# Kernel optimization log

Hardware: AMD Instinct MI355X
Metric: run time of the kernel (lower is better)

## Reference

```python
import jax, jax.numpy as jnp
import numpy as np

N_CODEBOOKS = 4
CODEBOOK_SIZE = 1024
CODEBOOK_DIM = 8
INPUT_DIM = 512
EPS_NORM = 1e-12  # F.normalize eps
EPS_SCALE = 1e-8


def _normalize(x, eps=EPS_NORM):
    n = jnp.linalg.norm(x, axis=-1, keepdims=True)
    return x / jnp.maximum(n, eps)


def _wn_weight(v, g):
    # weight-norm 1x1 conv weight: v [out, in], g [out]
    return g[:, None] * v / jnp.maximum(jnp.linalg.norm(v, axis=1, keepdims=True), EPS_NORM)


def _vq_step(residual, v_in, g_in, b_in, v_out, g_out, b_out, cb):
    # residual: [B, D, T]
    sg = jax.lax.stop_gradient
    w_in = _wn_weight(v_in, g_in)                                   # [cd, D]
    z_e = jnp.einsum('od,bdt->bot', w_in, residual) + b_in[None, :, None]  # [B, cd, T]

    # nearest-code search on L2-normalized vectors (same argmin as the cdist form)
    enc = jnp.transpose(z_e, (0, 2, 1))                             # [B, T, cd]
    sim = jnp.einsum('btd,kd->btk', _normalize(enc), _normalize(cb))
    idx = jnp.argmax(sim, axis=-1)                                  # [B, T]
    q_tok = cb[idx]                                                 # [B, T, cd]
    z_q_pre = jnp.transpose(q_tok, (0, 2, 1))                       # [B, cd, T]

    commit = jnp.mean((z_e - sg(z_q_pre)) ** 2, axis=(1, 2))        # [B]
    codeb = jnp.mean((z_q_pre - sg(z_e)) ** 2, axis=(1, 2))         # [B]

    # rotation trick: z_q = scale * (I - 2 r r^T + 2 q_n e_n^T) z_e, R/scale stop-grad
    e = enc                                                         # [B, T, cd]
    e_n = sg(_normalize(e))
    q_n = sg(_normalize(q_tok))
    r = sg(_normalize(e_n + q_n))
    scale = sg(jnp.linalg.norm(q_tok, axis=-1, keepdims=True)
               / jnp.maximum(jnp.linalg.norm(e, axis=-1, keepdims=True), EPS_SCALE))
    re = jnp.sum(r * e, axis=-1, keepdims=True)
    ene = jnp.sum(e_n * e, axis=-1, keepdims=True)
    z_rot = scale * (e - 2.0 * r * re + 2.0 * q_n * ene)            # [B, T, cd]
    z_q = jnp.transpose(z_rot, (0, 2, 1))                           # [B, cd, T]

    w_out = _wn_weight(v_out, g_out)                                # [D, cd]
    z_q_i = jnp.einsum('od,bdt->bot', w_out, z_q) + b_out[None, :, None]  # [B, D, T]
    return z_q_i, commit, codeb, idx


def setup_inputs() -> dict:
    key = jax.random.key(0)
    ks = jax.random.split(key, 8)
    B, D, T = 16, INPUT_DIM, 4096
    nq, K, cd = N_CODEBOOKS, CODEBOOK_SIZE, CODEBOOK_DIM
    return {
        'z': jax.random.normal(ks[0], (B, D, T), dtype=jnp.float32),
        'in_proj_v': jax.random.normal(ks[1], (nq, cd, D), dtype=jnp.float32) * (1.0 / np.sqrt(D)),
        'in_proj_g': jnp.ones((nq, cd), dtype=jnp.float32),
        'in_proj_b': jnp.zeros((nq, cd), dtype=jnp.float32),
        'out_proj_v': jax.random.normal(ks[2], (nq, D, cd), dtype=jnp.float32) * (1.0 / np.sqrt(cd)),
        'out_proj_g': jnp.ones((nq, D), dtype=jnp.float32),
        'out_proj_b': jnp.zeros((nq, D), dtype=jnp.float32),
        'codebooks': jax.random.normal(ks[3], (nq, K, cd), dtype=jnp.float32),
    }


def reference(z, in_proj_v, in_proj_g, in_proj_b, out_proj_v, out_proj_g, out_proj_b, codebooks):
    # eval-mode RVQ forward: all N_CODEBOOKS codebooks active (mask all ones)
    z_q = jnp.zeros_like(z)
    residual = z
    commitment_loss = jnp.float32(0.0)
    codebook_loss = jnp.float32(0.0)
    codes = []
    for i in range(N_CODEBOOKS):
        z_q_i, commit_i, codeb_i, idx_i = _vq_step(
            residual, in_proj_v[i], in_proj_g[i], in_proj_b[i],
            out_proj_v[i], out_proj_g[i], out_proj_b[i], codebooks[i])
        z_q = z_q + z_q_i
        residual = residual - z_q_i
        commitment_loss = commitment_loss + jnp.mean(commit_i)
        codebook_loss = codebook_loss + jnp.mean(codeb_i)
        codes.append(idx_i)
    return z_q, jnp.stack(codes, axis=0), commitment_loss, codebook_loss
```

## Files before the change

kernel.cpp:

```cpp
#include <hip/hip_runtime.h>
#include <cstddef>

#define NQ 4
#define KCODES 1024
#define CD 8
#define DIM 512
#define BATCH 16
#define TLEN 4096
#define TT 16
#define RPAD 17
#define NTHREADS 512

#define WS_WIN  0
#define WS_WOUT (NQ * DIM * CD)
#define WS_CBN  (2 * NQ * DIM * CD)
#define OUT_ZQ 0
#define OUT_CODES ((size_t)BATCH * DIM * TLEN)
#define OUT_LOSS (OUT_CODES + (size_t)NQ * BATCH * TLEN)

__global__ void rvq_zero(float* out) {
  out[OUT_LOSS] = 0.f;
  out[OUT_LOSS + 1] = 0.f;
}

__global__ void rvq_prep(const float* __restrict__ inv, const float* __restrict__ ing,
                         const float* __restrict__ outv, const float* __restrict__ outg,
                         const float* __restrict__ cb, float* __restrict__ ws) {
  const int blk = blockIdx.x, tid = threadIdx.x;
  if (blk < 32) {
    const int i = blk >> 3, o = blk & 7;
    const float* v = inv + (size_t)(i * CD + o) * DIM;
    const float a = v[tid], b = v[tid + 256];
    float s = a * a + b * b;
    #pragma unroll
    for (int off = 32; off >= 1; off >>= 1) s += __shfl_xor(s, off);
    __shared__ float red[4];
    if ((tid & 63) == 0) red[tid >> 6] = s;
    __syncthreads();
    const float nrm = fmaxf(sqrtf(red[0] + red[1] + red[2] + red[3]), 1e-12f);
    const float g = ing[i * CD + o];
    ws[WS_WIN + (size_t)((i * DIM + tid) * CD) + o] = (g * a) / nrm;
    ws[WS_WIN + (size_t)((i * DIM + tid + 256) * CD) + o] = (g * b) / nrm;
  } else {
    const int rid = (blk - 32) * 256 + tid;
    if (rid < NQ * DIM) {
      const float* v = outv + (size_t)rid * CD;
      float vv[8]; float n2 = 0.f;
      #pragma unroll
      for (int o = 0; o < 8; ++o) { vv[o] = v[o]; n2 += vv[o] * vv[o]; }
      const float nrm = fmaxf(sqrtf(n2), 1e-12f);
      const float g = outg[rid];
      #pragma unroll
      for (int o = 0; o < 8; ++o) ws[WS_WOUT + (size_t)rid * CD + o] = (g * vv[o]) / nrm;
    } else {
      const int k = rid - NQ * DIM;
      const float* v = cb + (size_t)k * CD;
      float vv[8]; float n2 = 0.f;
      #pragma unroll
      for (int o = 0; o < 8; ++o) { vv[o] = v[o]; n2 += vv[o] * vv[o]; }
      const float nrm = fmaxf(sqrtf(n2), 1e-12f);
      #pragma unroll
      for (int o = 0; o < 8; ++o) ws[WS_CBN + (size_t)k * CD + o] = vv[o] / nrm;
    }
  }
}

__launch_bounds__(NTHREADS, 8)
__global__ void rvq_main(const float* __restrict__ z,
                         const float* __restrict__ b_in, const float* __restrict__ b_out,
                         const float* __restrict__ cb, const float* __restrict__ ws,
                         float* __restrict__ out) {
  __shared__ float res[DIM * RPAD];
  __shared__ float part[8 * TT * 9];
  __shared__ float sc[8 * TT];
  __shared__ int   idl[8 * TT];

  const int tid = threadIdx.x;
  const int bb = blockIdx.x >> 8;
  const int t0 = (blockIdx.x & 255) * TT;
  const float* zb = z + (size_t)bb * DIM * TLEN + t0;

  {
    const int q = tid & 3, d0 = tid >> 2;
    #pragma unroll
    for (int p = 0; p < 4; ++p) {
      const int d = d0 + p * 128;
      const float4 v = *(const float4*)(zb + (size_t)d * TLEN + q * 4);
      float* rp = res + d * RPAD + q * 4;
      rp[0] = v.x; rp[1] = v.y; rp[2] = v.z; rp[3] = v.w;
    }
  }
  __syncthreads();

  const int t  = tid & 15;
  const int dc = tid >> 4;
  const int w  = tid >> 6;
  float loss_acc = 0.f;

  for (int i = 0; i < NQ; ++i) {
    float acc[8] = {0,0,0,0,0,0,0,0};
    {
      const float* wp = ws + WS_WIN + (size_t)(i * DIM + dc * 16) * CD;
      const float* rp = res + dc * 16 * RPAD + t;
      #pragma unroll
      for (int j = 0; j < 16; ++j) {
        const float r = rp[j * RPAD];
        const float4 w0 = *(const float4*)(wp + j * 8);
        const float4 w1 = *(const float4*)(wp + j * 8 + 4);
        acc[0] += w0.x * r; acc[1] += w0.y * r; acc[2] += w0.z * r; acc[3] += w0.w * r;
        acc[4] += w1.x * r; acc[5] += w1.y * r; acc[6] += w1.z * r; acc[7] += w1.w * r;
      }
    }
    #pragma unroll
    for (int o = 0; o < 8; ++o) {
      acc[o] += __shfl_xor(acc[o], 16);
      acc[o] += __shfl_xor(acc[o], 32);
    }
    if ((tid & 63) < 16) {
      float* pp = part + (w * TT + t) * 9;
      #pragma unroll
      for (int o = 0; o < 8; ++o) pp[o] = acc[o];
    }
    __syncthreads();

    float e[8];
    #pragma unroll
    for (int o = 0; o < 8; ++o) e[o] = b_in[i * CD + o];
    #pragma unroll
    for (int w2 = 0; w2 < 8; ++w2) {
      const float* pp = part + (w2 * TT + t) * 9;
      #pragma unroll
      for (int o = 0; o < 8; ++o) e[o] += pp[o];
    }
    float ne2 = 0.f;
    #pragma unroll
    for (int o = 0; o < 8; ++o) ne2 += e[o] * e[o];
    const float ne = sqrtf(ne2);

    float best = -1e30f; int bk = 0;
    {
      const float* cp = ws + WS_CBN + (size_t)(i * KCODES + dc * 32) * CD;
      #pragma unroll 4
      for (int k = 0; k < 32; ++k) {
        const float4 c0 = *(const float4*)(cp + k * 8);
        const float4 c1 = *(const float4*)(cp + k * 8 + 4);
        const float s = e[0]*c0.x + e[1]*c0.y + e[2]*c0.z + e[3]*c0.w
                      + e[4]*c1.x + e[5]*c1.y + e[6]*c1.z + e[7]*c1.w;
        if (s > best) { best = s; bk = dc * 32 + k; }
      }
    }
    #pragma unroll
    for (int off = 16; off <= 32; off <<= 1) {
      const float s2 = __shfl_xor(best, off);
      const int   k2 = __shfl_xor(bk, off);
      if (s2 > best || (s2 == best && k2 < bk)) { best = s2; bk = k2; }
    }
    if ((tid & 63) < 16) { sc[w * TT + t] = best; idl[w * TT + t] = bk; }
    __syncthreads();
    best = -1e30f; bk = KCODES;
    #pragma unroll
    for (int w2 = 0; w2 < 8; ++w2) {
      const float s2 = sc[w2 * TT + t];
      const int   k2 = idl[w2 * TT + t];
      if (s2 > best || (s2 == best && k2 < bk)) { best = s2; bk = k2; }
    }
    if (tid < TT) {
      out[OUT_CODES + (size_t)(i * BATCH + bb) * TLEN + t0 + tid] = (float)bk;
    }

    float qv[8];
    {
      const float* qp = cb + (size_t)(i * KCODES + bk) * CD;
      const float4 q0 = *(const float4*)qp;
      const float4 q1 = *(const float4*)(qp + 4);
      qv[0]=q0.x; qv[1]=q0.y; qv[2]=q0.z; qv[3]=q0.w;
      qv[4]=q1.x; qv[5]=q1.y; qv[6]=q1.z; qv[7]=q1.w;
    }
    if (dc == 0) {
      float s = 0.f;
      #pragma unroll
      for (int o = 0; o < 8; ++o) { const float d2 = e[o] - qv[o]; s += d2 * d2; }
      loss_acc += s;
    }

    const float rne = 1.f / fmaxf(ne, 1e-12f);
    float nq2 = 0.f;
    #pragma unroll
    for (int o = 0; o < 8; ++o) nq2 += qv[o] * qv[o];
    const float nq = sqrtf(nq2);
    const float rq = 1.f / fmaxf(nq, 1e-12f);
    float ru[8]; float nr2 = 0.f;
    #pragma unroll
    for (int o = 0; o < 8; ++o) { ru[o] = e[o] * rne + qv[o] * rq; nr2 += ru[o] * ru[o]; }
    const float rr = 1.f / fmaxf(sqrtf(nr2), 1e-12f);
    const float scale = nq / fmaxf(ne, 1e-8f);
    float re = 0.f;
    #pragma unroll
    for (int o = 0; o < 8; ++o) { ru[o] *= rr; re += ru[o] * e[o]; }
    const float ene = ne2 * rne;
    #pragma unroll
    for (int o = 0; o < 8; ++o)
      e[o] = scale * (e[o] - 2.f * ru[o] * re + 2.f * (qv[o] * rq) * ene);

    {
      const float* wp2 = ws + WS_WOUT + (size_t)(i * DIM + dc * 16) * CD;
      const float* bp2 = b_out + i * DIM + dc * 16;
      float* rp2 = res + dc * 16 * RPAD + t;
      #pragma unroll
      for (int j = 0; j < 16; ++j) {
        const float4 w0 = *(const float4*)(wp2 + j * 8);
        const float4 w1 = *(const float4*)(wp2 + j * 8 + 4);
        float v = bp2[j];
        v += w0.x*e[0] + w0.y*e[1] + w0.z*e[2] + w0.w*e[3]
           + w1.x*e[4] + w1.y*e[5] + w1.z*e[6] + w1.w*e[7];
        rp2[j * RPAD] -= v;
      }
    }
    __syncthreads();
  }

  {
    const int q = tid & 3, d0 = tid >> 2;
    float* ob = out + OUT_ZQ + (size_t)bb * DIM * TLEN + t0;
    #pragma unroll
    for (int p = 0; p < 4; ++p) {
      const int d = d0 + p * 128;
      float4 v = *(const float4*)(zb + (size_t)d * TLEN + q * 4);
      const float* rp = res + d * RPAD + q * 4;
      v.x -= rp[0]; v.y -= rp[1]; v.z -= rp[2]; v.w -= rp[3];
      *(float4*)(ob + (size_t)d * TLEN + q * 4) = v;
    }
  }

  loss_acc += __shfl_xor(loss_acc, 8);
  loss_acc += __shfl_xor(loss_acc, 4);
  loss_acc += __shfl_xor(loss_acc, 2);
  loss_acc += __shfl_xor(loss_acc, 1);
  if (tid == 0) {
    const float lv = loss_acc * (1.f / ((float)CD * TLEN * BATCH));
    atomicAdd(out + OUT_LOSS, lv);
    atomicAdd(out + OUT_LOSS + 1, lv);
  }
}

extern "C" void kernel_launch(void* const* d_in, const int* in_sizes, int n_in,
                              void* d_out, int out_size, void* d_ws, size_t ws_size,
                              hipStream_t stream) {
  const float* z    = (const float*)d_in[0];
  const float* inv  = (const float*)d_in[1];
  const float* ing  = (const float*)d_in[2];
  const float* inb  = (const float*)d_in[3];
  const float* outv = (const float*)d_in[4];
  const float* outg = (const float*)d_in[5];
  const float* outb = (const float*)d_in[6];
  const float* cbp  = (const float*)d_in[7];
  float* out = (float*)d_out;
  float* ws  = (float*)d_ws;

  hipLaunchKernelGGL(rvq_zero, dim3(1), dim3(1), 0, stream, out);
  hipLaunchKernelGGL(rvq_prep, dim3(56), dim3(256), 0, stream,
                     inv, ing, outv, outg, cbp, ws);
  hipLaunchKernelGGL(rvq_main, dim3(BATCH * (TLEN / TT)), dim3(NTHREADS),
                     0, stream, z, inb, outb, cbp, ws, out);
}
```

Measured before the change: 818.0 us.

## Restructure RVQ into low-rank latent recursion with separate in/out projection kernels

```diff
diff --git a/kernel.cpp b/kernel.cpp
--- a/kernel.cpp
+++ b/kernel.cpp
@@ -7,239 +7,291 @@
 #define DIM 512
 #define BATCH 16
 #define TLEN 4096
-#define TT 16
-#define RPAD 17
-#define NTHREADS 512
-
-#define WS_WIN  0
-#define WS_WOUT (NQ * DIM * CD)
-#define WS_CBN  (2 * NQ * DIM * CD)
+
 #define OUT_ZQ 0
 #define OUT_CODES ((size_t)BATCH * DIM * TLEN)
 #define OUT_LOSS (OUT_CODES + (size_t)NQ * BATCH * TLEN)
 
+#define WS_WT 0
+#define WS_WC 16384
+#define WS_CN 32768
+#define WS_M64 65536
+#define WS_CC64 67584
+#define WS_BS 67648
+#define WS_P  68160
+#define WS_ZR (WS_P + (size_t)BATCH * TLEN * 32)
+
 __global__ void rvq_zero(float* out) {
   out[OUT_LOSS] = 0.f;
   out[OUT_LOSS + 1] = 0.f;
 }
 
-__global__ void rvq_prep(const float* __restrict__ inv, const float* __restrict__ ing,
-                         const float* __restrict__ outv, const float* __restrict__ outg,
-                         const float* __restrict__ cb, float* __restrict__ ws) {
+__global__ void rvq_prep1(const float* __restrict__ inv, const float* __restrict__ ing,
+                          const float* __restrict__ outv, const float* __restrict__ outg,
+                          const float* __restrict__ cb, float* __restrict__ ws) {
   const int blk = blockIdx.x, tid = threadIdx.x;
   if (blk < 32) {
     const int i = blk >> 3, o = blk & 7;
     const float* v = inv + (size_t)(i * CD + o) * DIM;
     const float a = v[tid], b = v[tid + 256];
-    float s = a * a + b * b;
+    double s = (double)a * a + (double)b * b;
     #pragma unroll
     for (int off = 32; off >= 1; off >>= 1) s += __shfl_xor(s, off);
-    __shared__ float red[4];
+    __shared__ double red[4];
     if ((tid & 63) == 0) red[tid >> 6] = s;
     __syncthreads();
-    const float nrm = fmaxf(sqrtf(red[0] + red[1] + red[2] + red[3]), 1e-12f);
-    const float g = ing[i * CD + o];
-    ws[WS_WIN + (size_t)((i * DIM + tid) * CD) + o] = (g * a) / nrm;
-    ws[WS_WIN + (size_t)((i * DIM + tid + 256) * CD) + o] = (g * b) / nrm;
+    const double nrm = fmax(sqrt(red[0] + red[1] + red[2] + red[3]), 1e-12);
+    const double g = (double)ing[i * CD + o];
+    ws[WS_WT + (size_t)tid * 32 + i * 8 + o] = (float)(g * a / nrm);
+    ws[WS_WT + (size_t)(tid + 256) * 32 + i * 8 + o] = (float)(g * b / nrm);
   } else {
     const int rid = (blk - 32) * 256 + tid;
     if (rid < NQ * DIM) {
+      const int j = rid >> 9, d = rid & 511;
       const float* v = outv + (size_t)rid * CD;
-      float vv[8]; float n2 = 0.f;
-      #pragma unroll
-      for (int o = 0; o < 8; ++o) { vv[o] = v[o]; n2 += vv[o] * vv[o]; }
-      const float nrm = fmaxf(sqrtf(n2), 1e-12f);
-      const float g = outg[rid];
-      #pragma unroll
-      for (int o = 0; o < 8; ++o) ws[WS_WOUT + (size_t)rid * CD + o] = (g * vv[o]) / nrm;
+      float vv[8]; double n2 = 0.0;
+      #pragma unroll
+      for (int o = 0; o < 8; ++o) { vv[o] = v[o]; n2 += (double)vv[o] * vv[o]; }
+      const double nrm = fmax(sqrt(n2), 1e-12);
+      const double g = (double)outg[rid];
+      #pragma unroll
+      for (int o = 0; o < 8; ++o)
+        ws[WS_WC + (size_t)d * 32 + j * 8 + o] = (float)(g * vv[o] / nrm);
     } else {
       const int k = rid - NQ * DIM;
       const float* v = cb + (size_t)k * CD;
-      float vv[8]; float n2 = 0.f;
-      #pragma unroll
-      for (int o = 0; o < 8; ++o) { vv[o] = v[o]; n2 += vv[o] * vv[o]; }
-      const float nrm = fmaxf(sqrtf(n2), 1e-12f);
-      #pragma unroll
-      for (int o = 0; o < 8; ++o) ws[WS_CBN + (size_t)k * CD + o] = vv[o] / nrm;
-    }
-  }
-}
-
-__launch_bounds__(NTHREADS, 8)
-__global__ void rvq_main(const float* __restrict__ z,
-                         const float* __restrict__ b_in, const float* __restrict__ b_out,
-                         const float* __restrict__ cb, const float* __restrict__ ws,
-                         float* __restrict__ out) {
-  __shared__ float res[DIM * RPAD];
-  __shared__ float part[8 * TT * 9];
-  __shared__ float sc[8 * TT];
-  __shared__ int   idl[8 * TT];
-
-  const int tid = threadIdx.x;
-  const int bb = blockIdx.x >> 8;
-  const int t0 = (blockIdx.x & 255) * TT;
-  const float* zb = z + (size_t)bb * DIM * TLEN + t0;
-
+      float vv[8]; double n2 = 0.0;
+      #pragma unroll
+      for (int o = 0; o < 8; ++o) { vv[o] = v[o]; n2 += (double)vv[o] * vv[o]; }
+      const double nrm = fmax(sqrt(n2), 1e-12);
+      #pragma unroll
+      for (int o = 0; o < 8; ++o)
+        ws[WS_CN + (size_t)k * 8 + o] = (float)(vv[o] / nrm);
+    }
+  }
+}
+
+__global__ void rvq_prep2(const float* __restrict__ inb, const float* __restrict__ outb,
+                          float* __restrict__ ws) {
+  double* m64  = (double*)(ws + WS_M64);
+  double* cc64 = (double*)(ws + WS_CC64);
+  const int gid = blockIdx.x * 256 + threadIdx.x;
+  if (gid < 1024) {
+    const int i = gid >> 8, j = (gid >> 6) & 3, o = (gid >> 3) & 7, oo = gid & 7;
+    double m = 0.0;
+    if (j < i) {
+      const float* wt = ws + WS_WT + i * 8 + o;
+      const float* wc = ws + WS_WC + j * 8 + oo;
+      for (int d = 0; d < DIM; ++d)
+        m += (double)wt[(size_t)d * 32] * (double)wc[(size_t)d * 32];
+    }
+    m64[gid] = m;
+  } else if (gid < 1056) {
+    const int t2 = gid - 1024, i = t2 >> 3, o = t2 & 7;
+    double c = (double)inb[i * CD + o];
+    const float* wt = ws + WS_WT + i * 8 + o;
+    for (int j = 0; j < i; ++j) {
+      const float* bo = outb + (size_t)j * DIM;
+      double s = 0.0;
+      for (int d = 0; d < DIM; ++d) s += (double)wt[(size_t)d * 32] * (double)bo[d];
+      c -= s;
+    }
+    cc64[t2] = c;
+  } else if (gid < 1568) {
+    const int d = gid - 1056;
+    float s = 0.f;
+    #pragma unroll
+    for (int j = 0; j < NQ; ++j) s += outb[(size_t)j * DIM + d];
+    ws[WS_BS + d] = s;
+  }
+}
+
+__launch_bounds__(256)
+__global__ void rvq_inproj(const float* __restrict__ z, const float* __restrict__ wsc,
+                           float* __restrict__ ws) {
+  const int blk = blockIdx.x, tid = threadIdx.x;
+  const int b = blk >> 5, t0 = (blk & 31) * 128;
+  const int hid = tid >> 7, t = tid & 127;
+  const float* zp = z + (size_t)b * DIM * TLEN + t0 + t;
+  const float* wt = wsc + WS_WT + hid * 16;
+  double a64[16];
+  #pragma unroll
+  for (int o = 0; o < 16; ++o) a64[o] = 0.0;
+  for (int c = 0; c < 16; ++c) {
+    float a32[16];
+    #pragma unroll
+    for (int o = 0; o < 16; ++o) a32[o] = 0.f;
+    #pragma unroll 8
+    for (int dd = 0; dd < 32; ++dd) {
+      const int d = c * 32 + dd;
+      const float zv = zp[(size_t)d * TLEN];
+      #pragma unroll
+      for (int o = 0; o < 16; ++o) a32[o] += wt[(size_t)d * 32 + o] * zv;
+    }
+    #pragma unroll
+    for (int o = 0; o < 16; ++o) a64[o] += (double)a32[o];
+  }
+  float* pw = ws + WS_P + ((size_t)b * TLEN + t0 + t) * 32 + hid * 16;
+  #pragma unroll
+  for (int q = 0; q < 4; ++q)
+    *(float4*)(pw + q * 4) = make_float4((float)a64[q*4], (float)a64[q*4+1],
+                                         (float)a64[q*4+2], (float)a64[q*4+3]);
+}
+
+__launch_bounds__(256)
+__global__ void rvq_latent(const float* __restrict__ cb, const float* __restrict__ wsc,
+                           float* __restrict__ ws, float* __restrict__ out) {
+  const int blk = blockIdx.x, tid = threadIdx.x;
+  const int b = blk >> 4, t0 = (blk & 15) * 256;
+  const size_t g = (size_t)b * TLEN + t0 + tid;
+  const double* m64  = (const double*)(wsc + WS_M64);
+  const double* cc64 = (const double*)(wsc + WS_CC64);
+
+  double p64[32];
   {
-    const int q = tid & 3, d0 = tid >> 2;
-    #pragma unroll
-    for (int p = 0; p < 4; ++p) {
-      const int d = d0 + p * 128;
-      const float4 v = *(const float4*)(zb + (size_t)d * TLEN + q * 4);
-      float* rp = res + d * RPAD + q * 4;
-      rp[0] = v.x; rp[1] = v.y; rp[2] = v.z; rp[3] = v.w;
-    }
-  }
-  __syncthreads();
-
-  const int t  = tid & 15;
-  const int dc = tid >> 4;
-  const int w  = tid >> 6;
-  float loss_acc = 0.f;
-
+    const float* pp = ws + WS_P + g * 32;
+    #pragma unroll
+    for (int q = 0; q < 8; ++q) {
+      const float4 v = *(const float4*)(pp + q * 4);
+      p64[q*4] = v.x; p64[q*4+1] = v.y; p64[q*4+2] = v.z; p64[q*4+3] = v.w;
+    }
+  }
+  double loss64 = 0.0;
+
+  #pragma unroll
   for (int i = 0; i < NQ; ++i) {
-    float acc[8] = {0,0,0,0,0,0,0,0};
-    {
-      const float* wp = ws + WS_WIN + (size_t)(i * DIM + dc * 16) * CD;
-      const float* rp = res + dc * 16 * RPAD + t;
-      #pragma unroll
-      for (int j = 0; j < 16; ++j) {
-        const float r = rp[j * RPAD];
-        const float4 w0 = *(const float4*)(wp + j * 8);
-        const float4 w1 = *(const float4*)(wp + j * 8 + 4);
-        acc[0] += w0.x * r; acc[1] += w0.y * r; acc[2] += w0.z * r; acc[3] += w0.w * r;
-        acc[4] += w1.x * r; acc[5] += w1.y * r; acc[6] += w1.z * r; acc[7] += w1.w * r;
+    float e32[8];
+    #pragma unroll
+    for (int o = 0; o < 8; ++o) e32[o] = (float)(p64[i * 8 + o] + cc64[i * 8 + o]);
+
+    float ne2f = 0.f;
+    #pragma unroll
+    for (int o = 0; o < 8; ++o) ne2f += e32[o] * e32[o];
+    const float den = fmaxf(sqrtf(ne2f), 1e-12f);
+    float en[8];
+    #pragma unroll
+    for (int o = 0; o < 8; ++o) en[o] = e32[o] / den;
+
+    const float* cn = wsc + WS_CN + (size_t)i * KCODES * 8;
+    float best = -1e30f; int bk = 0;
+    for (int k0 = 0; k0 < KCODES; k0 += 4) {
+      float s0 = 0.f, s1 = 0.f, s2 = 0.f, s3 = 0.f;
+      const float* c0 = cn + (size_t)k0 * 8;
+      #pragma unroll
+      for (int o = 0; o < 8; ++o) {
+        s0 += c0[o]      * en[o];
+        s1 += c0[8 + o]  * en[o];
+        s2 += c0[16 + o] * en[o];
+        s3 += c0[24 + o] * en[o];
       }
-    }
-    #pragma unroll
-    for (int o = 0; o < 8; ++o) {
-      acc[o] += __shfl_xor(acc[o], 16);
-      acc[o] += __shfl_xor(acc[o], 32);
-    }
-    if ((tid & 63) < 16) {
-      float* pp = part + (w * TT + t) * 9;
-      #pragma unroll
-      for (int o = 0; o < 8; ++o) pp[o] = acc[o];
-    }
-    __syncthreads();
-
-    float e[8];
-    #pragma unroll
-    for (int o = 0; o < 8; ++o) e[o] = b_in[i * CD + o];
-    #pragma unroll
-    for (int w2 = 0; w2 < 8; ++w2) {
-      const float* pp = part + (w2 * TT + t) * 9;
-      #pragma unroll
-      for (int o = 0; o < 8; ++o) e[o] += pp[o];
-    }
-    float ne2 = 0.f;
-    #pragma unroll
-    for (int o = 0; o < 8; ++o) ne2 += e[o] * e[o];
-    const float ne = sqrtf(ne2);
-
-    float best = -1e30f; int bk = 0;
-    {
-      const float* cp = ws + WS_CBN + (size_t)(i * KCODES + dc * 32) * CD;
-      #pragma unroll 4
-      for (int k = 0; k < 32; ++k) {
-        const float4 c0 = *(const float4*)(cp + k * 8);
-        const float4 c1 = *(const float4*)(cp + k * 8 + 4);
-        const float s = e[0]*c0.x + e[1]*c0.y + e[2]*c0.z + e[3]*c0.w
-                      + e[4]*c1.x + e[5]*c1.y + e[6]*c1.z + e[7]*c1.w;
-        if (s > best) { best = s; bk = dc * 32 + k; }
-      }
-    }
-    #pragma unroll
-    for (int off = 16; off <= 32; off <<= 1) {
-      const float s2 = __shfl_xor(best, off);
-      const int   k2 = __shfl_xor(bk, off);
-      if (s2 > best || (s2 == best && k2 < bk)) { best = s2; bk = k2; }
-    }
-    if ((tid & 63) < 16) { sc[w * TT + t] = best; idl[w * TT + t] = bk; }
-    __syncthreads();
-    best = -1e30f; bk = KCODES;
-    #pragma unroll
-    for (int w2 = 0; w2 < 8; ++w2) {
-      const float s2 = sc[w2 * TT + t];
-      const int   k2 = idl[w2 * TT + t];
-      if (s2 > best || (s2 == best && k2 < bk)) { best = s2; bk = k2; }
-    }
-    if (tid < TT) {
-      out[OUT_CODES + (size_t)(i * BATCH + bb) * TLEN + t0 + tid] = (float)bk;
-    }
+      if (s0 > best) { best = s0; bk = k0; }
+      if (s1 > best) { best = s1; bk = k0 + 1; }
+      if (s2 > best) { best = s2; bk = k0 + 2; }
+      if (s3 > best) { best = s3; bk = k0 + 3; }
+    }
+    out[OUT_CODES + (size_t)(i * BATCH + b) * TLEN + t0 + tid] = (float)bk;
 
     float qv[8];
     {
-      const float* qp = cb + (size_t)(i * KCODES + bk) * CD;
+      const float* qp = cb + (size_t)(i * KCODES + bk) * 8;
       const float4 q0 = *(const float4*)qp;
       const float4 q1 = *(const float4*)(qp + 4);
       qv[0]=q0.x; qv[1]=q0.y; qv[2]=q0.z; qv[3]=q0.w;
       qv[4]=q1.x; qv[5]=q1.y; qv[6]=q1.z; qv[7]=q1.w;
     }
-    if (dc == 0) {
-      float s = 0.f;
-      #pragma unroll
-      for (int o = 0; o < 8; ++o) { const float d2 = e[o] - qv[o]; s += d2 * d2; }
-      loss_acc += s;
-    }
-
-    const float rne = 1.f / fmaxf(ne, 1e-12f);
-    float nq2 = 0.f;
-    #pragma unroll
-    for (int o = 0; o < 8; ++o) nq2 += qv[o] * qv[o];
-    const float nq = sqrtf(nq2);
-    const float rq = 1.f / fmaxf(nq, 1e-12f);
-    float ru[8]; float nr2 = 0.f;
-    #pragma unroll
-    for (int o = 0; o < 8; ++o) { ru[o] = e[o] * rne + qv[o] * rq; nr2 += ru[o] * ru[o]; }
-    const float rr = 1.f / fmaxf(sqrtf(nr2), 1e-12f);
-    const float scale = nq / fmaxf(ne, 1e-8f);
-    float re = 0.f;
-    #pragma unroll
-    for (int o = 0; o < 8; ++o) { ru[o] *= rr; re += ru[o] * e[o]; }
-    const float ene = ne2 * rne;
+    #pragma unroll
+    for (int o = 0; o < 8; ++o) {
+      const double d2 = (double)e32[o] - (double)qv[o];
+      loss64 += d2 * d2;
+    }
+    double ne64 = 0.0, nq64 = 0.0;
+    #pragma unroll
+    for (int o = 0; o < 8; ++o) {
+      ne64 += (double)e32[o] * e32[o];
+      nq64 += (double)qv[o] * qv[o];
+    }
+    const double ne_d = sqrt(ne64), nq_d = sqrt(nq64);
+    const double rne = 1.0 / fmax(ne_d, 1e-12);
+    const double rq  = 1.0 / fmax(nq_d, 1e-12);
+    double ru[8]; double nr2 = 0.0;
+    #pragma unroll
+    for (int o = 0; o < 8; ++o) {
+      ru[o] = (double)e32[o] * rne + (double)qv[o] * rq;
+      nr2 += ru[o] * ru[o];
+    }
+    const double rr = 1.0 / fmax(sqrt(nr2), 1e-12);
+    const double scale = nq_d / fmax(ne_d, 1e-8);
+    double re = 0.0;
+    #pragma unroll
+    for (int o = 0; o < 8; ++o) { ru[o] *= rr; re += ru[o] * (double)e32[o]; }
+    const double ene = ne64 * rne;
+    double zr64[8];
     #pragma unroll
     for (int o = 0; o < 8; ++o)
-      e[o] = scale * (e[o] - 2.f * ru[o] * re + 2.f * (qv[o] * rq) * ene);
+      zr64[o] = scale * ((double)e32[o] - 2.0 * ru[o] * re + 2.0 * ((double)qv[o] * rq) * ene);
 
     {
-      const float* wp2 = ws + WS_WOUT + (size_t)(i * DIM + dc * 16) * CD;
-      const float* bp2 = b_out + i * DIM + dc * 16;
-      float* rp2 = res + dc * 16 * RPAD + t;
-      #pragma unroll
-      for (int j = 0; j < 16; ++j) {
-        const float4 w0 = *(const float4*)(wp2 + j * 8);
-        const float4 w1 = *(const float4*)(wp2 + j * 8 + 4);
-        float v = bp2[j];
-        v += w0.x*e[0] + w0.y*e[1] + w0.z*e[2] + w0.w*e[3]
-           + w1.x*e[4] + w1.y*e[5] + w1.z*e[6] + w1.w*e[7];
-        rp2[j * RPAD] -= v;
+      float* zw = ws + WS_ZR + g * 32 + i * 8;
+      *(float4*)zw       = make_float4((float)zr64[0], (float)zr64[1], (float)zr64[2], (float)zr64[3]);
+      *(float4*)(zw + 4) = make_float4((float)zr64[4], (float)zr64[5], (float)zr64[6], (float)zr64[7]);
+    }
+    #pragma unroll
+    for (int i2 = i + 1; i2 < NQ; ++i2) {
+      const double* mp = m64 + (size_t)(i2 * 4 + i) * 64;
+      #pragma unroll
+      for (int o = 0; o < 8; ++o) {
+        double s = 0.0;
+        #pragma unroll
+        for (int oo = 0; oo < 8; ++oo) s += mp[o * 8 + oo] * zr64[oo];
+        p64[i2 * 8 + o] -= s;
       }
     }
-    __syncthreads();
-  }
-
-  {
-    const int q = tid & 3, d0 = tid >> 2;
-    float* ob = out + OUT_ZQ + (size_t)bb * DIM * TLEN + t0;
-    #pragma unroll
-    for (int p = 0; p < 4; ++p) {
-      const int d = d0 + p * 128;
-      float4 v = *(const float4*)(zb + (size_t)d * TLEN + q * 4);
-      const float* rp = res + d * RPAD + q * 4;
-      v.x -= rp[0]; v.y -= rp[1]; v.z -= rp[2]; v.w -= rp[3];
-      *(float4*)(ob + (size_t)d * TLEN + q * 4) = v;
-    }
-  }
-
-  loss_acc += __shfl_xor(loss_acc, 8);
-  loss_acc += __shfl_xor(loss_acc, 4);
-  loss_acc += __shfl_xor(loss_acc, 2);
-  loss_acc += __shfl_xor(loss_acc, 1);
-  if (tid == 0) {
-    const float lv = loss_acc * (1.f / ((float)CD * TLEN * BATCH));
+  }
+
+  #pragma unroll
+  for (int off = 32; off >= 1; off >>= 1) loss64 += __shfl_xor(loss64, off);
+  if ((tid & 63) == 0) {
+    const float lv = (float)(loss64 * (1.0 / ((double)CD * TLEN * BATCH)));
     atomicAdd(out + OUT_LOSS, lv);
     atomicAdd(out + OUT_LOSS + 1, lv);
+  }
+}
+
+__launch_bounds__(256)
+__global__ void rvq_outproj(const float* __restrict__ wsc, const float* __restrict__ ws,
+                            float* __restrict__ out) {
+  const int blk = blockIdx.x, tid = threadIdx.x;
+  const int b = blk >> 5, rem = blk & 31;
+  const int d0 = (rem >> 3) * 128, t0 = (rem & 7) * 512;
+  const int t = t0 + 2 * tid;
+  const size_t g = (size_t)b * TLEN + t;
+
+  float za[32], zb2[32];
+  {
+    const float* zp = ws + WS_ZR + g * 32;
+    #pragma unroll
+    for (int q = 0; q < 8; ++q) {
+      const float4 v = *(const float4*)(zp + q * 4);
+      za[q*4] = v.x; za[q*4+1] = v.y; za[q*4+2] = v.z; za[q*4+3] = v.w;
+      const float4 w = *(const float4*)(zp + 32 + q * 4);
+      zb2[q*4] = w.x; zb2[q*4+1] = w.y; zb2[q*4+2] = w.z; zb2[q*4+3] = w.w;
+    }
+  }
+  const float* wc = wsc + WS_WC;
+  const float* bs = wsc + WS_BS;
+  float* ob = out + OUT_ZQ + (size_t)b * DIM * TLEN + t;
+  #pragma unroll 2
+  for (int dr = 0; dr < 128; ++dr) {
+    const int d = d0 + dr;
+    const float* wp = wc + (size_t)d * 32;
+    float a0 = bs[d], a1 = a0;
+    #pragma unroll
+    for (int o = 0; o < 32; ++o) {
+      const float w = wp[o];
+      a0 += w * za[o];
+      a1 += w * zb2[o];
+    }
+    *(float2*)(ob + (size_t)d * TLEN) = make_float2(a0, a1);
   }
 }
 
@@ -257,9 +309,10 @@
   float* out = (float*)d_out;
   float* ws  = (float*)d_ws;
 
-  hipLaunchKernelGGL(rvq_zero, dim3(1), dim3(1), 0, stream, out);
-  hipLaunchKernelGGL(rvq_prep, dim3(56), dim3(256), 0, stream,
-                     inv, ing, outv, outg, cbp, ws);
-  hipLaunchKernelGGL(rvq_main, dim3(BATCH * (TLEN / TT)), dim3(NTHREADS),
-                     0, stream, z, inb, outb, cbp, ws, out);
-}
+  hipLaunchKernelGGL(rvq_zero,   dim3(1),   dim3(1),   0, stream, out);
+  hipLaunchKernelGGL(rvq_prep1,  dim3(56),  dim3(256), 0, stream, inv, ing, outv, outg, cbp, ws);
+  hipLaunchKernelGGL(rvq_prep2,  dim3(8),   dim3(256), 0, stream, inb, outb, ws);
+  hipLaunchKernelGGL(rvq_inproj, dim3(512), dim3(256), 0, stream, z, ws, ws);
+  hipLaunchKernelGGL(rvq_latent, dim3(256), dim3(256), 0, stream, cbp, ws, ws, out);
+  hipLaunchKernelGGL(rvq_outproj,dim3(512), dim3(256), 0, stream, ws, ws, out);
+}
```

New measurement: 937.4 us. +14.6%, slower.
